# Kernel tuning notes

Measured on AMD Instinct MI355X. Metric: run time of the kernel, lower is better.

The kernel has to match this reference:

```python
import jax, jax.numpy as jnp
import numpy as np

EMBED_DIM = 1024
HEAD_DIM = 128


def setup_inputs() -> dict:
    key = jax.random.key(0)
    k_x, k_qkv, k_out, k_b = jax.random.split(key, 4)
    x = jax.random.normal(k_x, (4, 4096, EMBED_DIM), dtype=jnp.float32)
    # torch Linear weights, stored as [in, out] so y = x @ W
    w_qkv = jax.random.normal(k_qkv, (EMBED_DIM, 3 * HEAD_DIM), dtype=jnp.float32) * (EMBED_DIM ** -0.5)
    w_out = jax.random.normal(k_out, (HEAD_DIM, EMBED_DIM), dtype=jnp.float32) * (HEAD_DIM ** -0.5)
    b_out = jax.random.normal(k_b, (EMBED_DIM,), dtype=jnp.float32) * 0.01
    return {"x": x, "w_qkv": w_qkv, "w_out": w_out, "b_out": b_out}


def reference(x, w_qkv, w_out, b_out):
    b, t, c = x.shape
    qkv = x @ w_qkv                                  # [b, t, 3*head_dim]
    q, k, v = jnp.split(qkv, 3, axis=-1)             # each [b, t, head_dim]
    # NOTE: original scales by embed_dim**-0.5 (c), not head_dim**-0.5
    wei = jnp.einsum('bqd,bkd->bqk', q, k) * (c ** -0.5)  # [b, t, t]
    causal = jnp.tril(jnp.ones((t, t), dtype=bool))
    wei = jnp.where(causal, wei, -jnp.inf)
    wei = jax.nn.softmax(wei, axis=-1)
    out = jnp.einsum('bqk,bkd->bqd', wei, v)         # [b, t, head_dim]
    return out @ w_out + b_out                       # [b, t, embed_dim]
```

## Files before the change

### kernel.cpp

```cpp
#include <hip/hip_runtime.h>
#include <hip/hip_bf16.h>

typedef __attribute__((ext_vector_type(8))) short short8;
typedef __attribute__((ext_vector_type(4))) float float4v;

#define AS1(p) ((const __attribute__((address_space(1))) void*)(p))
#define AS3(p) ((__attribute__((address_space(3))) void*)(p))

#define NSPLIT 8

__device__ __forceinline__ ushort f2bf(float f) {
    union { float f; unsigned u; } v; v.f = f;
    unsigned u = v.u;
    unsigned r = (u + 0x7fffu + ((u >> 16) & 1u)) >> 16;
    return (ushort)r;
}
__device__ __forceinline__ ushort f2bf_trunc(float f) {
    union { float f; unsigned u; } v; v.f = f;
    return (ushort)(v.u >> 16);
}
__device__ __forceinline__ float bf2f(ushort u) {
    union { unsigned u; float f; } v; v.u = ((unsigned)u) << 16;
    return v.f;
}

__global__ void transpose_cast(const float* __restrict__ in, ushort* __restrict__ out, int R, int C) {
    int idx = blockIdx.x * blockDim.x + threadIdx.x;
    if (idx >= R * C) return;
    int r = idx / C, c = idx - r * C;
    out[(size_t)c * R + r] = f2bf(in[idx]);
}

__device__ __forceinline__ void stage128x64(const ushort* gbase, int ld, ushort* lds, int tid) {
    const int wavebase = tid & 192;
#pragma unroll
    for (int j = 0; j < 4; ++j) {
        int idx = j * 256 + tid;
        int row = idx >> 3;
        int slot = idx & 7;
        int s = slot ^ (row & 7);
        const ushort* g = gbase + (size_t)row * ld + s * 8;
        int ldsoff = (j * 256 + wavebase) * 16;
        __builtin_amdgcn_global_load_lds(AS1(g), AS3((char*)lds + ldsoff), 16, 0, 0);
    }
}

__device__ __forceinline__ void compute64(const ushort* As, const ushort* Bs,
                                          int wr, int wc, int row16, int grp,
                                          float4v acc[4][4]) {
    const char* Ab = (const char*)As;
    const char* Bb = (const char*)Bs;
#pragma unroll
    for (int kk = 0; kk < 2; ++kk) {
        short8 a[4], b[4];
        const int sw = row16 & 7;
#pragma unroll
        for (int m = 0; m < 4; ++m)
            a[m] = *(const short8*)(Ab + (wr * 64 + m * 16 + row16) * 128 + (((kk * 4 + grp) ^ sw) << 4));
#pragma unroll
        for (int n = 0; n < 4; ++n)
            b[n] = *(const short8*)(Bb + (wc * 64 + n * 16 + row16) * 128 + (((kk * 4 + grp) ^ sw) << 4));
#pragma unroll
        for (int m = 0; m < 4; ++m)
#pragma unroll
            for (int n = 0; n < 4; ++n)
                acc[m][n] = __builtin_amdgcn_mfma_f32_16x16x32_bf16(a[m], b[n], acc[m][n], 0, 0, 0);
    }
}

__global__ __launch_bounds__(256) void gemm_qkv(const float* __restrict__ x,
                                                const ushort* __restrict__ wT,
                                                ushort* __restrict__ Qm,
                                                ushort* __restrict__ Km,
                                                ushort* __restrict__ Vt) {
    __shared__ ushort S[17408];
    ushort* As = S;
    ushort* Bs = S + 8192;
    const int tid = threadIdx.x;
    const int lane = tid & 63, w = tid >> 6;
    const int row16 = lane & 15, grp = lane >> 4;
    const int wr = w >> 1, wc = w & 1;
    const int mt = blockIdx.x * 128;
    const int by = blockIdx.y;
    const int n0 = by * 128;

    float4v acc[4][4];
#pragma unroll
    for (int m = 0; m < 4; ++m)
#pragma unroll
        for (int n = 0; n < 4; ++n) acc[m][n] = (float4v){0.f, 0.f, 0.f, 0.f};

    for (int kt = 0; kt < 1024; kt += 64) {
        stage128x64(wT + (size_t)n0 * 1024 + kt, 1024, Bs, tid);
        float4 va[4][2];
#pragma unroll
        for (int j = 0; j < 4; ++j) {
            int idx = j * 256 + tid;
            int row = idx >> 3, slot = idx & 7;
            const float* src = x + (size_t)(mt + row) * 1024 + kt + slot * 8;
            va[j][0] = *(const float4*)(src);
            va[j][1] = *(const float4*)(src + 4);
        }
#pragma unroll
        for (int j = 0; j < 4; ++j) {
            int idx = j * 256 + tid;
            int row = idx >> 3, slot = idx & 7;
            short8 h;
            h[0] = f2bf(va[j][0].x); h[1] = f2bf(va[j][0].y);
            h[2] = f2bf(va[j][0].z); h[3] = f2bf(va[j][0].w);
            h[4] = f2bf(va[j][1].x); h[5] = f2bf(va[j][1].y);
            h[6] = f2bf(va[j][1].z); h[7] = f2bf(va[j][1].w);
            *(short8*)((char*)As + row * 128 + ((slot ^ (row & 7)) << 4)) = h;
        }
        __syncthreads();
        compute64(As, Bs, wr, wc, row16, grp, acc);
        __syncthreads();
    }

    if (by == 2) {
#pragma unroll
        for (int m = 0; m < 4; ++m)
#pragma unroll
            for (int i = 0; i < 4; ++i) {
                int trow = wr * 64 + m * 16 + grp * 4 + i;
#pragma unroll
                for (int n = 0; n < 4; ++n) {
                    int d = wc * 64 + n * 16 + row16;
                    S[d * 136 + trow] = f2bf(acc[m][n][i]);
                }
            }
        __syncthreads();
        const int b = mt >> 12, tloc = mt & 4095;
#pragma unroll
        for (int j = 0; j < 8; ++j) {
            int chunk = j * 256 + tid;
            int d = chunk >> 4, tc = chunk & 15;
            *(short8*)(Vt + ((size_t)(b * 128 + d)) * 4096 + tloc + tc * 8) =
                *(const short8*)(S + d * 136 + tc * 8);
        }
        return;
    }

    const float oscale = (by == 0) ? (0.03125f * 1.44269504f) : 1.0f;
    ushort* dst = (by == 0) ? Qm : Km;
#pragma unroll
    for (int m = 0; m < 4; ++m)
#pragma unroll
        for (int i = 0; i < 4; ++i) {
            int row = mt + wr * 64 + m * 16 + grp * 4 + i;
#pragma unroll
            for (int n = 0; n < 4; ++n) {
                int coll = wc * 64 + n * 16 + row16;
                dst[(size_t)row * 128 + coll] = f2bf(acc[m][n][i] * oscale);
            }
        }
}

__global__ __launch_bounds__(256, 3) void attn_split(const ushort* __restrict__ Qm,
                                                     const ushort* __restrict__ Km,
                                                     const ushort* __restrict__ Vt,
                                                     ushort* __restrict__ Opart,
                                                     float* __restrict__ Lpart) {
    __shared__ ushort Ks[2][32 * 128];
    __shared__ ushort Vs[2][128 * 32];
    __shared__ ushort Ps[4][32 * 32];

    const int tid = threadIdx.x;
    const int lane = tid & 63, w = tid >> 6;
    const int row16 = lane & 15, grp = lane >> 4;

    const int bx = blockIdx.x;
    const int xcd = bx & 7;
    const int b = xcd >> 1;
    const int combo = ((bx >> 3) << 1) | (xcd & 1);
    const int qb = 31 - (combo >> 3);
    const int s = combo & 7;

    const int ext = 4 * qb + 4;
    const int t0 = (s * ext) >> 3;
    const int t1 = ((s + 1) * ext) >> 3;

    const int qtile32 = qb * 4 + w;
    const int qt0 = qtile32 * 32;
    const int qmax = qt0 + 31;
    const size_t pbase = ((size_t)b * 128 + qtile32) * NSPLIT + s;
    float* mlL = Lpart + pbase * 32;

    if (t0 >= t1) {
        if (lane < 32) mlL[lane] = 0.f;
        return;
    }

    const ushort* qbp = Qm + ((size_t)(b * 4096 + qt0 + row16)) * 128 + grp * 8;
    short8 qf[2][4];
#pragma unroll
    for (int rt = 0; rt < 2; ++rt)
#pragma unroll
        for (int kk = 0; kk < 4; ++kk)
            qf[rt][kk] = *reinterpret_cast<const short8*>(qbp + rt * 16 * 128 + kk * 32);

    float4v o[2][8];
#pragma unroll
    for (int rt = 0; rt < 2; ++rt)
#pragma unroll
        for (int dt = 0; dt < 8; ++dt) o[rt][dt] = (float4v){0.f, 0.f, 0.f, 0.f};
    float lrun[2][4];
#pragma unroll
    for (int rt = 0; rt < 2; ++rt)
#pragma unroll
        for (int i = 0; i < 4; ++i) lrun[rt][i] = 0.f;

    const ushort* kbase = Km + (size_t)b * 4096 * 128;
    const ushort* vbase = Vt + (size_t)b * 128 * 4096;
    char* Pw = (char*)&Ps[w][0];

#define STAGE_KV(KVT, BUF)                                                                     \
    {                                                                                          \
        const ushort* kb_ = kbase + (size_t)(KVT) * 128;                                       \
        _Pragma("unroll") for (int j = 0; j < 2; ++j) {                                        \
            int idx = j * 256 + tid;                                                           \
            int row = idx >> 4, c = idx & 15;                                                  \
            int sc_ = (c & 8) | ((c & 7) ^ (row & 7));                                         \
            __builtin_amdgcn_global_load_lds(AS1(kb_ + (size_t)row * 128 + sc_ * 8),           \
                AS3((char*)&Ks[BUF][0] + (j * 256 + (tid & 192)) * 16), 16, 0, 0);             \
        }                                                                                      \
        const ushort* vb_ = vbase + (KVT);                                                     \
        _Pragma("unroll") for (int j = 0; j < 2; ++j) {                                        \
            int idx = j * 256 + tid;                                                           \
            int row = idx >> 2, c = idx & 3;                                                   \
            int sc_ = c ^ ((row >> 1) & 3);                                                    \
            __builtin_amdgcn_global_load_lds(AS1(vb_ + (size_t)row * 4096 + sc_ * 8),          \
                AS3((char*)&Vs[BUF][0] + (j * 256 + (tid & 192)) * 16), 16, 0, 0);             \
        }                                                                                      \
    }

    STAGE_KV(t0 * 32, 0);
    __syncthreads();

    int cur = 0;
    for (int t = t0; t < t1; ++t) {
        const int kvt = t * 32;
        if (t + 1 < t1) STAGE_KV((t + 1) * 32, cur ^ 1);

        if (kvt <= qmax) {
            float4v a[2][2];
#pragma unroll
            for (int rt = 0; rt < 2; ++rt)
#pragma unroll
                for (int ct = 0; ct < 2; ++ct) a[rt][ct] = (float4v){0.f, 0.f, 0.f, 0.f};
            const char* Kb = (const char*)&Ks[cur][0];
            __builtin_amdgcn_s_setprio(1);
#pragma unroll
            for (int ct = 0; ct < 2; ++ct) {
                int r0 = ct * 16 + row16;
                int rx = r0 & 7;
#pragma unroll
                for (int kk = 0; kk < 4; ++kk) {
                    int c = kk * 4 + grp;
                    int sc_ = (c & 8) | ((c & 7) ^ rx);
                    short8 kfr = *(const short8*)(Kb + r0 * 256 + sc_ * 16);
                    a[0][ct] = __builtin_amdgcn_mfma_f32_16x16x32_bf16(qf[0][kk], kfr, a[0][ct], 0, 0, 0);
                    a[1][ct] = __builtin_amdgcn_mfma_f32_16x16x32_bf16(qf[1][kk], kfr, a[1][ct], 0, 0, 0);
                }
            }
            __builtin_amdgcn_s_setprio(0);
            if (kvt + 31 > qt0) {
#pragma unroll
                for (int ct = 0; ct < 2; ++ct) {
                    int kcol = kvt + ct * 16 + row16;
#pragma unroll
                    for (int rt = 0; rt < 2; ++rt)
#pragma unroll
                        for (int i = 0; i < 4; ++i) {
                            int q = qt0 + rt * 16 + grp * 4 + i;
                            if (kcol > q) a[rt][ct][i] = -3e38f;
                        }
                }
            }
#pragma unroll
            for (int rt = 0; rt < 2; ++rt)
#pragma unroll
                for (int i = 0; i < 4; ++i) {
#pragma unroll
                    for (int ct = 0; ct < 2; ++ct) {
                        float p = exp2f(a[rt][ct][i]);
                        a[rt][ct][i] = p;
                        lrun[rt][i] += p;
                    }
                }
#pragma unroll
            for (int rt = 0; rt < 2; ++rt)
#pragma unroll
                for (int ct = 0; ct < 2; ++ct)
#pragma unroll
                    for (int i = 0; i < 4; ++i) {
                        int r = rt * 16 + grp * 4 + i;
                        int chunk = (ct * 2 + (row16 >> 3)) ^ ((r >> 1) & 3);
                        *(ushort*)(Pw + r * 64 + (chunk << 4) + ((row16 & 7) << 1)) = f2bf_trunc(a[rt][ct][i]);
                    }
            const char* Vb = (const char*)&Vs[cur][0];
            __builtin_amdgcn_s_setprio(1);
            {
                short8 pa0 = *(const short8*)(Pw + row16 * 64 + ((grp ^ ((row16 >> 1) & 3)) << 4));
                short8 pa1 = *(const short8*)(Pw + (16 + row16) * 64 + ((grp ^ (((16 + row16) >> 1) & 3)) << 4));
#pragma unroll
                for (int dt = 0; dt < 8; ++dt) {
                    int r = dt * 16 + row16;
                    int sc_ = grp ^ ((r >> 1) & 3);
                    short8 vfr = *(const short8*)(Vb + r * 64 + sc_ * 16);
                    o[0][dt] = __builtin_amdgcn_mfma_f32_16x16x32_bf16(pa0, vfr, o[0][dt], 0, 0, 0);
                    o[1][dt] = __builtin_amdgcn_mfma_f32_16x16x32_bf16(pa1, vfr, o[1][dt], 0, 0, 0);
                }
            }
            __builtin_amdgcn_s_setprio(0);
        }
        __syncthreads();
        cur ^= 1;
    }
#undef STAGE_KV

#pragma unroll
    for (int rt = 0; rt < 2; ++rt)
#pragma unroll
        for (int i = 0; i < 4; ++i) {
            float psum = lrun[rt][i];
#pragma unroll
            for (int msk = 1; msk < 16; msk <<= 1) psum += __shfl_xor(psum, msk);
            lrun[rt][i] = psum;
        }
    ushort* ob = Opart + pbase * 32 * 128;
#pragma unroll
    for (int rt = 0; rt < 2; ++rt)
#pragma unroll
        for (int i = 0; i < 4; ++i) {
            int r = rt * 16 + grp * 4 + i;
#pragma unroll
            for (int dt = 0; dt < 8; ++dt)
                ob[(size_t)r * 128 + dt * 16 + row16] = f2bf(o[rt][dt][i]);
        }
    if (row16 == 0) {
#pragma unroll
        for (int rt = 0; rt < 2; ++rt)
#pragma unroll
            for (int i = 0; i < 4; ++i)
                mlL[rt * 16 + grp * 4 + i] = lrun[rt][i];
    }
}

__global__ __launch_bounds__(128) void attn_combine(const ushort* __restrict__ Opart,
                                                    const float* __restrict__ Lpart,
                                                    ushort* __restrict__ AO) {
    const int row = blockIdx.x;
    const int b = row >> 12, t = row & 4095;
    const int qtile = t >> 5, r = t & 31;
    const size_t sb = (((size_t)b * 128 + qtile) * NSPLIT);
    const int col = threadIdx.x;
    float acc = 0.f, denom = 0.f;
#pragma unroll
    for (int s = 0; s < NSPLIT; ++s) {
        float l = Lpart[(sb + s) * 32 + r];
        if (l > 0.f) {
            denom += l;
            acc += bf2f(Opart[((sb + s) * 32 + r) * 128 + col]);
        }
    }
    AO[(size_t)row * 128 + col] = f2bf(acc / denom);
}

__global__ __launch_bounds__(256) void gemm_out(const ushort* __restrict__ AO,
                                                const ushort* __restrict__ wT,
                                                const float* __restrict__ bias,
                                                float* __restrict__ out) {
    __shared__ ushort As[128 * 64];
    __shared__ ushort Bs[128 * 64];
    const int tid = threadIdx.x;
    const int lane = tid & 63, w = tid >> 6;
    const int row16 = lane & 15, grp = lane >> 4;
    const int wr = w >> 1, wc = w & 1;
    const int mt = blockIdx.x * 128;
    const int n0 = blockIdx.y * 128;

    float4v acc[4][4];
#pragma unroll
    for (int m = 0; m < 4; ++m)
#pragma unroll
        for (int n = 0; n < 4; ++n) acc[m][n] = (float4v){0.f, 0.f, 0.f, 0.f};

#pragma unroll
    for (int kt = 0; kt < 128; kt += 64) {
        stage128x64(AO + (size_t)mt * 128 + kt, 128, As, tid);
        stage128x64(wT + (size_t)n0 * 128 + kt, 128, Bs, tid);
        __syncthreads();
        compute64(As, Bs, wr, wc, row16, grp, acc);
        __syncthreads();
    }

#pragma unroll
    for (int n = 0; n < 4; ++n) {
        int col = n0 + wc * 64 + n * 16 + row16;
        float bv = bias[col];
#pragma unroll
        for (int m = 0; m < 4; ++m)
#pragma unroll
            for (int i = 0; i < 4; ++i) {
                int row = mt + wr * 64 + m * 16 + grp * 4 + i;
                out[(size_t)row * 1024 + col] = acc[m][n][i] + bv;
            }
    }
}

extern "C" void kernel_launch(void* const* d_in, const int* in_sizes, int n_in,
                              void* d_out, int out_size, void* d_ws, size_t ws_size,
                              hipStream_t stream) {
    const float* x     = (const float*)d_in[0];
    const float* w_qkv = (const float*)d_in[1];
    const float* w_out = (const float*)d_in[2];
    const float* b_out = (const float*)d_in[3];
    float* out = (float*)d_out;

    char* ws = (char*)d_ws;
    ushort* wqkvT = (ushort*)(ws + 33554432);
    ushort* woutT = (ushort*)(ws + 34340864);
    ushort* Qm    = (ushort*)(ws + 34603008);
    ushort* Km    = (ushort*)(ws + 38797312);
    ushort* Vt    = (ushort*)(ws + 42991616);
    ushort* AO    = (ushort*)(ws + 47185920);
    ushort* Opart = (ushort*)(ws);
    float* Lpart  = (float*)(ws + 51380224);

    transpose_cast<<<dim3((1024 * 384 + 255) / 256), dim3(256), 0, stream>>>(w_qkv, wqkvT, 1024, 384);
    transpose_cast<<<dim3((128 * 1024 + 255) / 256), dim3(256), 0, stream>>>(w_out, woutT, 128, 1024);

    gemm_qkv<<<dim3(128, 3), dim3(256), 0, stream>>>(x, wqkvT, Qm, Km, Vt);

    attn_split<<<dim3(1024), dim3(256), 0, stream>>>(Qm, Km, Vt, Opart, Lpart);
    attn_combine<<<dim3(16384), dim3(128), 0, stream>>>(Opart, Lpart, AO);

    gemm_out<<<dim3(128, 8), dim3(256), 0, stream>>>(AO, woutT, b_out, out);
}
```

Baseline: 114.8 us.

## Halve QKV GEMM M-tile to 64 rows and prefetch next x tile into registers

The QKV projection GEMM now uses 64-row M tiles instead of 128, which doubles the grid to 768 blocks to fill the GPU's compute units better, and shrinks shared memory. It also software-pipelines the fp32 x loads, issuing the next K-slice's global loads before the MFMA compute of the current slice. The cost is less reuse of each weight tile per block, since W is re-staged twice as often, and fewer MFMAs per LDS load.

```diff
diff --git a/kernel.cpp b/kernel.cpp
--- a/kernel.cpp
+++ b/kernel.cpp
@@ -68,41 +68,67 @@
     }
 }
 
+__device__ __forceinline__ void compute64x128(const ushort* As, const ushort* Bs,
+                                              int wr, int wc, int row16, int grp,
+                                              float4v acc[2][4]) {
+    const char* Ab = (const char*)As;
+    const char* Bb = (const char*)Bs;
+#pragma unroll
+    for (int kk = 0; kk < 2; ++kk) {
+        short8 a[2], b[4];
+        const int sw = row16 & 7;
+#pragma unroll
+        for (int m = 0; m < 2; ++m)
+            a[m] = *(const short8*)(Ab + (wr * 32 + m * 16 + row16) * 128 + (((kk * 4 + grp) ^ sw) << 4));
+#pragma unroll
+        for (int n = 0; n < 4; ++n)
+            b[n] = *(const short8*)(Bb + (wc * 64 + n * 16 + row16) * 128 + (((kk * 4 + grp) ^ sw) << 4));
+#pragma unroll
+        for (int m = 0; m < 2; ++m)
+#pragma unroll
+            for (int n = 0; n < 4; ++n)
+                acc[m][n] = __builtin_amdgcn_mfma_f32_16x16x32_bf16(a[m], b[n], acc[m][n], 0, 0, 0);
+    }
+}
+
 __global__ __launch_bounds__(256) void gemm_qkv(const float* __restrict__ x,
                                                 const ushort* __restrict__ wT,
                                                 ushort* __restrict__ Qm,
                                                 ushort* __restrict__ Km,
                                                 ushort* __restrict__ Vt) {
-    __shared__ ushort S[17408];
+    __shared__ ushort S[12288];
     ushort* As = S;
-    ushort* Bs = S + 8192;
+    ushort* Bs = S + 4096;
     const int tid = threadIdx.x;
     const int lane = tid & 63, w = tid >> 6;
     const int row16 = lane & 15, grp = lane >> 4;
     const int wr = w >> 1, wc = w & 1;
-    const int mt = blockIdx.x * 128;
+    const int mt = blockIdx.x * 64;
     const int by = blockIdx.y;
     const int n0 = by * 128;
 
-    float4v acc[4][4];
-#pragma unroll
-    for (int m = 0; m < 4; ++m)
+    float4v acc[2][4];
+#pragma unroll
+    for (int m = 0; m < 2; ++m)
 #pragma unroll
         for (int n = 0; n < 4; ++n) acc[m][n] = (float4v){0.f, 0.f, 0.f, 0.f};
+
+#define LOAD_A(KT)                                                         \
+    _Pragma("unroll") for (int j = 0; j < 2; ++j) {                        \
+        int idx = j * 256 + tid;                                           \
+        int row = idx >> 3, slot = idx & 7;                                \
+        const float* src = x + (size_t)(mt + row) * 1024 + (KT) + slot * 8;\
+        va[j][0] = *(const float4*)(src);                                  \
+        va[j][1] = *(const float4*)(src + 4);                              \
+    }
+
+    float4 va[2][2];
+    LOAD_A(0);
 
     for (int kt = 0; kt < 1024; kt += 64) {
         stage128x64(wT + (size_t)n0 * 1024 + kt, 1024, Bs, tid);
-        float4 va[4][2];
-#pragma unroll
-        for (int j = 0; j < 4; ++j) {
-            int idx = j * 256 + tid;
-            int row = idx >> 3, slot = idx & 7;
-            const float* src = x + (size_t)(mt + row) * 1024 + kt + slot * 8;
-            va[j][0] = *(const float4*)(src);
-            va[j][1] = *(const float4*)(src + 4);
-        }
-#pragma unroll
-        for (int j = 0; j < 4; ++j) {
+#pragma unroll
+        for (int j = 0; j < 2; ++j) {
             int idx = j * 256 + tid;
             int row = idx >> 3, slot = idx & 7;
             short8 h;
@@ -113,30 +139,32 @@
             *(short8*)((char*)As + row * 128 + ((slot ^ (row & 7)) << 4)) = h;
         }
         __syncthreads();
-        compute64(As, Bs, wr, wc, row16, grp, acc);
-        __syncthreads();
-    }
+        if (kt + 64 < 1024) LOAD_A(kt + 64);
+        compute64x128(As, Bs, wr, wc, row16, grp, acc);
+        __syncthreads();
+    }
+#undef LOAD_A
 
     if (by == 2) {
 #pragma unroll
-        for (int m = 0; m < 4; ++m)
+        for (int m = 0; m < 2; ++m)
 #pragma unroll
             for (int i = 0; i < 4; ++i) {
-                int trow = wr * 64 + m * 16 + grp * 4 + i;
+                int trow = wr * 32 + m * 16 + grp * 4 + i;
 #pragma unroll
                 for (int n = 0; n < 4; ++n) {
                     int d = wc * 64 + n * 16 + row16;
-                    S[d * 136 + trow] = f2bf(acc[m][n][i]);
+                    S[d * 72 + trow] = f2bf(acc[m][n][i]);
                 }
             }
         __syncthreads();
         const int b = mt >> 12, tloc = mt & 4095;
 #pragma unroll
-        for (int j = 0; j < 8; ++j) {
+        for (int j = 0; j < 4; ++j) {
             int chunk = j * 256 + tid;
-            int d = chunk >> 4, tc = chunk & 15;
+            int d = chunk >> 3, tc = chunk & 7;
             *(short8*)(Vt + ((size_t)(b * 128 + d)) * 4096 + tloc + tc * 8) =
-                *(const short8*)(S + d * 136 + tc * 8);
+                *(const short8*)(S + d * 72 + tc * 8);
         }
         return;
     }
@@ -144,10 +172,10 @@
     const float oscale = (by == 0) ? (0.03125f * 1.44269504f) : 1.0f;
     ushort* dst = (by == 0) ? Qm : Km;
 #pragma unroll
-    for (int m = 0; m < 4; ++m)
+    for (int m = 0; m < 2; ++m)
 #pragma unroll
         for (int i = 0; i < 4; ++i) {
-            int row = mt + wr * 64 + m * 16 + grp * 4 + i;
+            int row = mt + wr * 32 + m * 16 + grp * 4 + i;
 #pragma unroll
             for (int n = 0; n < 4; ++n) {
                 int coll = wc * 64 + n * 16 + row16;
@@ -431,7 +459,7 @@
     transpose_cast<<<dim3((1024 * 384 + 255) / 256), dim3(256), 0, stream>>>(w_qkv, wqkvT, 1024, 384);
     transpose_cast<<<dim3((128 * 1024 + 255) / 256), dim3(256), 0, stream>>>(w_out, woutT, 128, 1024);
 
-    gemm_qkv<<<dim3(128, 3), dim3(256), 0, stream>>>(x, wqkvT, Qm, Km, Vt);
+    gemm_qkv<<<dim3(256, 3), dim3(256), 0, stream>>>(x, wqkvT, Qm, Km, Vt);
 
     attn_split<<<dim3(1024), dim3(256), 0, stream>>>(Qm, Km, Vt, Opart, Lpart);
     attn_combine<<<dim3(16384), dim3(128), 0, stream>>>(Opart, Lpart, AO);
```

Result: faster. 108.6 us (-5.4%).
